# Performance work log

Measured on AMD Instinct MI355X. Metric: run time of the kernel, lower is better.

## Reference

```python
import jax, jax.numpy as jnp
import numpy as np

B, C, H, W = 8, 512, 32, 32
NUM_HEADS = 8
WINDOW = 32
L = H * W
BN_EPS = 1e-5


def setup_inputs() -> dict:
    key = jax.random.key(0)
    ks = jax.random.split(key, 8)
    s = lambda k, shape, sc=0.02: jax.random.normal(k, shape, jnp.float32) * sc
    return {
        "x": jax.random.normal(ks[0], (B, C, H, W), jnp.float32),
        "dw_weight": s(ks[1], (C, 1, 3, 3), 0.1),
        "dw_bias": jnp.zeros((C,), jnp.float32),
        "shared_weight": s(ks[2], (1, 1, 3, 3), 0.3),
        "shared_bias": jnp.zeros((1,), jnp.float32),
        "mix_weight": jnp.float32(0.7),
        "bn_gamma": jnp.ones((C,), jnp.float32),
        "bn_beta": jnp.zeros((C,), jnp.float32),
        "det_w1": s(ks[3], (C // 4, 2 * C)),
        "det_b1": jnp.zeros((C // 4,), jnp.float32),
        "det_w2": s(ks[4], (1, C // 4)),
        "det_b2": jnp.zeros((1,), jnp.float32),
        "in_proj_w": s(ks[5], (3 * C, C)),
        "in_proj_b": jnp.zeros((3 * C,), jnp.float32),
        "out_proj_w": s(ks[6], (C, C)),
        "out_proj_b": jnp.zeros((C,), jnp.float32),
    }


def _circ_pad(x):
    # F.pad(x, (1,1,1,1), mode='circular')
    return jnp.pad(x, ((0, 0), (0, 0), (1, 1), (1, 1)), mode="wrap")


def _dw_conv(xp, w, b):
    # depthwise 3x3, VALID on circularly padded input
    out = jax.lax.conv_general_dilated(
        xp, w, window_strides=(1, 1), padding="VALID",
        dimension_numbers=("NCHW", "OIHW", "NCHW"), feature_group_count=C)
    return out + b[None, :, None, None]


def _local_mask():
    # True = blocked; row i allows columns [i - WINDOW//2, i + WINDOW//2]
    i = jnp.arange(L)[:, None]
    j = jnp.arange(L)[None, :]
    allowed = (j >= i - WINDOW // 2) & (j <= i + WINDOW // 2)
    return ~allowed


def _forward(x, dw_weight, dw_bias, shared_weight, shared_bias, mix_weight,
             bn_gamma, bn_beta, det_w1, det_b1, det_w2, det_b2,
             in_proj_w, in_proj_b, out_proj_w, out_proj_b):
    # --- DualWalze (eval mode: BN uses running_mean=0, running_var=1) ---
    xp = _circ_pad(x)
    main_out = _dw_conv(xp, dw_weight, dw_bias)
    shared_kernel = jnp.broadcast_to(shared_weight, (C, 1, 3, 3))
    shared_b = jnp.broadcast_to(shared_bias, (C,))
    express_out = _dw_conv(xp, shared_kernel, shared_b)
    mix = jax.nn.sigmoid(mix_weight)
    combined = mix * main_out + (1.0 - mix) * express_out + x  # residual
    bn = bn_gamma[None, :, None, None] * combined * jax.lax.rsqrt(jnp.float32(1.0 + BN_EPS)) \
         + bn_beta[None, :, None, None]
    x_walze = jax.nn.gelu(bn, approximate=False)  # (B, C, H, W)

    # --- AdaptiveSpikeDetectorV3 (eval: no history, temp = 1.0) ---
    x_before_seq = x.transpose(0, 2, 3, 1).reshape(B, L, C)
    x_after_seq = x_walze.transpose(0, 2, 3, 1).reshape(B, L, C)
    comb = jnp.concatenate([x_before_seq, x_after_seq], axis=-1)  # (B, L, 2C)
    h = jax.nn.gelu(jnp.einsum("blf,kf->blk", comb, det_w1) + det_b1, approximate=False)
    spike_logits = jnp.einsum("blk,ok->blo", h, det_w2) + det_b2  # (B, L, 1)
    soft_mask = jax.nn.sigmoid(spike_logits)  # temperature 1.0 at progress 0
    soft_mask = soft_mask.reshape(B, H, W, 1).transpose(0, 3, 1, 2)  # (B,1,H,W)

    # --- AttentionWithMemory: windowed MHA over flattened sequence ---
    seq = x_after_seq  # (B, L, C)
    qkv = jnp.einsum("blc,fc->blf", seq, in_proj_w) + in_proj_b
    q, k, v = jnp.split(qkv, 3, axis=-1)
    hd = C // NUM_HEADS
    to_heads = lambda t: t.reshape(B, L, NUM_HEADS, hd).transpose(0, 2, 1, 3)
    q, k, v = to_heads(q), to_heads(k), to_heads(v)
    scores = jnp.einsum("bhqd,bhkd->bhqk", q, k) / jnp.sqrt(jnp.float32(hd))
    scores = jnp.where(_local_mask()[None, None], jnp.float32(-1e30), scores)
    attn = jax.nn.softmax(scores, axis=-1)
    ctx = jnp.einsum("bhqk,bhkd->bhqd", attn, v)
    ctx = ctx.transpose(0, 2, 1, 3).reshape(B, L, C)
    attn_out = jnp.einsum("blc,oc->blo", ctx, out_proj_w) + out_proj_b
    attn_spatial = attn_out.reshape(B, H, W, C).transpose(0, 3, 1, 2)

    # --- gated residual combine ---
    return x_walze + soft_mask * attn_spatial


def reference(x, dw_weight, dw_bias, shared_weight, shared_bias, mix_weight,
              bn_gamma, bn_beta, det_w1, det_b1, det_w2, det_b2,
              in_proj_w, in_proj_b, out_proj_w, out_proj_b):
    return _forward(x, dw_weight, dw_bias, shared_weight, shared_bias, mix_weight,
                    bn_gamma, bn_beta, det_w1, det_b1, det_w2, det_b2,
                    in_proj_w, in_proj_b, out_proj_w, out_proj_b)
```

## Files before the change

kernel.cpp:

```cpp
#include <hip/hip_runtime.h>

#define B_ 8
#define C_ 512
#define H_ 32
#define W_ 32
#define L_ 1024
#define M_ 8192
#define NH_ 8
#define HD_ 64

typedef float f32x4 __attribute__((ext_vector_type(4)));
typedef short s16x8 __attribute__((ext_vector_type(8)));

__device__ __forceinline__ f32x4 mfma_bf16(f32x4 acc, s16x8 a, s16x8 b) {
    asm("v_mfma_f32_16x16x32_bf16 %0, %1, %2, %0" : "+v"(acc) : "v"(a), "v"(b));
    return acc;
}

__device__ __forceinline__ s16x8 ldg8(const unsigned short* p) {
    return *(const s16x8*)p;
}

typedef __attribute__((address_space(1))) const unsigned int glob_u32;
typedef __attribute__((address_space(3))) unsigned int lds_u32;
__device__ __forceinline__ void async_cp16(const void* g, void* l) {
    __builtin_amdgcn_global_load_lds((glob_u32*)g, (lds_u32*)l, 16, 0, 0);
}

__device__ __forceinline__ unsigned short f2bf(float f) {
    unsigned int u = __float_as_uint(f);
    unsigned int r = (u + 0x7FFFu + ((u >> 16) & 1u)) >> 16;
    return (unsigned short)r;
}

__device__ __forceinline__ float bf2f(unsigned short u) {
    return __uint_as_float(((unsigned int)u) << 16);
}

__device__ __forceinline__ float gelu_exact(float v) {
    return 0.5f * v * (1.0f + erff(v * 0.70710678118654752f));
}

__device__ __forceinline__ float sigmoidf_(float v) {
    return 1.0f / (1.0f + __expf(-v));
}

__global__ __launch_bounds__(256) void k_cvt_weights(
        const float* __restrict__ w1, const float* __restrict__ w2,
        const float* __restrict__ w3,
        unsigned short* __restrict__ o1, unsigned short* __restrict__ o2,
        unsigned short* __restrict__ o3, int n1, int n2, int n3) {
    int i = blockIdx.x * 256 + threadIdx.x;
    if (i < n1) o1[i] = f2bf(w1[i]);
    if (i < n2) o2[i] = f2bf(w2[i]);
    if (i < n3) o3[i] = f2bf(w3[i]);
}

__global__ __launch_bounds__(256) void k_walze(
        const float* __restrict__ x, const float* __restrict__ dww,
        const float* __restrict__ dwb, const float* __restrict__ shw,
        const float* __restrict__ shb, const float* __restrict__ mixw,
        const float* __restrict__ gamma, const float* __restrict__ beta,
        float* __restrict__ xw) {
    __shared__ float tile[1024];
    int bc = blockIdx.x;
    int c = bc & (C_ - 1);
    int tid = threadIdx.x;
    const float* xp = x + (size_t)bc * 1024;
#pragma unroll
    for (int t = 0; t < 4; ++t) tile[tid + 256 * t] = xp[tid + 256 * t];
    __syncthreads();
    float wm[9], wsh[9];
#pragma unroll
    for (int t = 0; t < 9; ++t) { wm[t] = dww[c * 9 + t]; wsh[t] = shw[t]; }
    float mix = sigmoidf_(mixw[0]);
    float bmain = dwb[c], bsh = shb[0];
    float g = gamma[c], bt = beta[c];
    const float rs = rsqrtf(1.0f + 1e-5f);
#pragma unroll
    for (int t = 0; t < 4; ++t) {
        int l = tid + 256 * t;
        int h = l >> 5, w = l & 31;
        float accm = 0.f, accs = 0.f;
#pragma unroll
        for (int kh = 0; kh < 3; ++kh) {
            int hh = (h + kh + 31) & 31;
#pragma unroll
            for (int kw = 0; kw < 3; ++kw) {
                int ww = (w + kw + 31) & 31;
                float v = tile[hh * 32 + ww];
                accm += v * wm[kh * 3 + kw];
                accs += v * wsh[kh * 3 + kw];
            }
        }
        float combined = mix * (accm + bmain) + (1.f - mix) * (accs + bsh) + tile[l];
        float bn = g * combined * rs + bt;
        xw[(size_t)bc * 1024 + l] = gelu_exact(bn);
    }
}

__global__ __launch_bounds__(256) void k_pack(
        const float* __restrict__ x, const float* __restrict__ xw,
        unsigned short* __restrict__ comb) {
    __shared__ float Tx[64 * 65];
    __shared__ float Tw[64 * 65];
    int b = blockIdx.z;
    int c0 = blockIdx.y * 64;
    int l0 = blockIdx.x * 64;
    int tid = threadIdx.x;
    for (int idx = tid; idx < 1024; idx += 256) {
        int cr = idx >> 4, f = idx & 15;
        size_t src = ((size_t)(b * C_ + c0 + cr) << 10) + l0 + f * 4;
        float4 vx = *(const float4*)(x + src);
        float4 vw = *(const float4*)(xw + src);
        *(float4*)&Tx[cr * 65 + f * 4] = vx;
        *(float4*)&Tw[cr * 65 + f * 4] = vw;
    }
    __syncthreads();
    for (int idx = tid; idx < 1024; idx += 256) {
        int lr = idx >> 4, f = idx & 15;
        ushort4 ux, uw;
        ux.x = f2bf(Tx[(4 * f + 0) * 65 + lr]);
        ux.y = f2bf(Tx[(4 * f + 1) * 65 + lr]);
        ux.z = f2bf(Tx[(4 * f + 2) * 65 + lr]);
        ux.w = f2bf(Tx[(4 * f + 3) * 65 + lr]);
        uw.x = f2bf(Tw[(4 * f + 0) * 65 + lr]);
        uw.y = f2bf(Tw[(4 * f + 1) * 65 + lr]);
        uw.z = f2bf(Tw[(4 * f + 2) * 65 + lr]);
        uw.w = f2bf(Tw[(4 * f + 3) * 65 + lr]);
        unsigned short* row = comb + (((size_t)(b << 10) + l0 + lr) << 10);
        *(ushort4*)(row + c0 + 4 * f) = ux;
        *(ushort4*)(row + 512 + c0 + 4 * f) = uw;
    }
}

__global__ __launch_bounds__(256) void k_detector(
        const unsigned short* __restrict__ comb, const unsigned short* __restrict__ w1,
        const float* __restrict__ b1, const float* __restrict__ w2,
        const float* __restrict__ b2, float* __restrict__ sm) {
    __shared__ float red[64];
    int tid = threadIdx.x;
    int wave = tid >> 6, lane = tid & 63;
    int col = lane & 15, quad = lane >> 4;
    int m0 = blockIdx.x * 16;
    int koff = quad * 8;
    int nb0 = wave * 32, nb1 = nb0 + 16;
    const unsigned short* pa  = comb + (size_t)(m0 + col) * 1024 + koff;
    const unsigned short* pw0 = w1 + (size_t)(nb0 + col) * 1024 + koff;
    const unsigned short* pw1 = w1 + (size_t)(nb1 + col) * 1024 + koff;
    f32x4 acc0 = {0.f, 0.f, 0.f, 0.f}, acc1 = {0.f, 0.f, 0.f, 0.f};
    for (int k = 0; k < 1024; k += 32) {
        s16x8 a = ldg8(pa + k);
        acc0 = mfma_bf16(acc0, a, ldg8(pw0 + k));
        acc1 = mfma_bf16(acc1, a, ldg8(pw1 + k));
    }
    asm volatile("s_nop 7\ns_nop 7");
    float bia0 = b1[nb0 + col], bia1 = b1[nb1 + col];
    float wv0 = w2[nb0 + col], wv1 = w2[nb1 + col];
#pragma unroll
    for (int r = 0; r < 4; ++r) {
        float h0 = gelu_exact(acc0[r] + bia0);
        float h1 = gelu_exact(acc1[r] + bia1);
        float p = h0 * wv0 + h1 * wv1;
        p += __shfl_xor(p, 1);
        p += __shfl_xor(p, 2);
        p += __shfl_xor(p, 4);
        p += __shfl_xor(p, 8);
        if (col == 0) red[wave * 16 + quad * 4 + r] = p;
    }
    __syncthreads();
    if (tid < 16) {
        float s = red[tid] + red[16 + tid] + red[32 + tid] + red[48 + tid] + b2[0];
        sm[m0 + tid] = sigmoidf_(s);
    }
}

__global__ __launch_bounds__(256) void k_gemm_qkv(
        const unsigned short* __restrict__ A,
        const unsigned short* __restrict__ Wt,
        const float* __restrict__ bias,
        unsigned short* __restrict__ out_hi, unsigned short* __restrict__ out_lo) {
    __shared__ unsigned short As[128 * 64];
    __shared__ unsigned short Bs[128 * 64];
    int tid = threadIdx.x;
    int wave = tid >> 6, lane = tid & 63;
    int col = lane & 15, quad = lane >> 4;
    int wr = wave & 1, wc = wave >> 1;
    int mb = blockIdx.y * 128, nb = blockIdx.x * 128;
    int srow = tid >> 3, sko = tid & 7;
    bool write_lo = (nb >= 1024);
    f32x4 acc[4][4] = {};
    for (int kb = 0; kb < 512; kb += 64) {
#pragma unroll
        for (int p = 0; p < 4; ++p) {
            int r = p * 32 + srow;
            async_cp16(A + (size_t)(mb + r) * 1024 + kb + sko * 8, &As[r * 64 + sko * 8]);
            async_cp16(Wt + (size_t)(nb + r) * 512 + kb + sko * 8, &Bs[r * 64 + sko * 8]);
        }
        __syncthreads();
#pragma unroll
        for (int ks = 0; ks < 64; ks += 32) {
            s16x8 a[4], b[4];
#pragma unroll
            for (int i = 0; i < 4; ++i)
                a[i] = *(const s16x8*)&As[(wr * 64 + i * 16 + col) * 64 + ks + quad * 8];
#pragma unroll
            for (int j = 0; j < 4; ++j)
                b[j] = *(const s16x8*)&Bs[(wc * 64 + j * 16 + col) * 64 + ks + quad * 8];
#pragma unroll
            for (int i = 0; i < 4; ++i)
#pragma unroll
                for (int j = 0; j < 4; ++j)
                    acc[i][j] = mfma_bf16(acc[i][j], a[i], b[j]);
        }
        __syncthreads();
    }
    asm volatile("s_nop 7\ns_nop 7");
#pragma unroll
    for (int i = 0; i < 4; ++i)
#pragma unroll
        for (int j = 0; j < 4; ++j) {
            int n = nb + wc * 64 + j * 16 + col;
            float bv = bias[n];
#pragma unroll
            for (int r = 0; r < 4; ++r) {
                int m = mb + wr * 64 + i * 16 + quad * 4 + r;
                float v = acc[i][j][r] + bv;
                unsigned short hi = f2bf(v);
                size_t idx = (size_t)m * 1536 + n;
                out_hi[idx] = hi;
                if (write_lo) out_lo[idx] = f2bf(v - bf2f(hi));
            }
        }
}

__global__ __launch_bounds__(256) void k_attn(
        const unsigned short* __restrict__ qkv_hi,
        const unsigned short* __restrict__ qkv_lo,
        unsigned short* __restrict__ ctx) {
    __shared__ unsigned short Vth[64 * 112];
    __shared__ unsigned short Vtl[64 * 112];
    __shared__ unsigned short Ph[4][16 * 72];
    __shared__ unsigned short Pl[4][16 * 72];
    int b = blockIdx.z, h = blockIdx.y;
    int q0 = blockIdx.x * 64;
    int tid = threadIdx.x, wave = tid >> 6, lane = tid & 63;
    int col = lane & 15, quad = lane >> 4;
    int jlo_t = max(q0 - 16, 0);
    const unsigned short* baseh = qkv_hi + ((size_t)(b << 10)) * 1536;
    const unsigned short* basel = qkv_lo + ((size_t)(b << 10)) * 1536;
#pragma unroll
    for (int it = 0; it < 3; ++it) {
        int slot = it * 256 + tid;
        int kg = slot >> 6, d = slot & 63;
        int key0 = jlo_t + kg * 8;
        unsigned short eh[8], el[8];
#pragma unroll
        for (int t = 0; t < 8; ++t) {
            size_t ro = (size_t)min(key0 + t, 1023) * 1536 + 1024 + h * 64 + d;
            eh[t] = baseh[ro];
            el[t] = basel[ro];
        }
        ushort4 h0 = {eh[0], eh[1], eh[2], eh[3]}, h1 = {eh[4], eh[5], eh[6], eh[7]};
        ushort4 l0 = {el[0], el[1], el[2], el[3]}, l1 = {el[4], el[5], el[6], el[7]};
        *(ushort4*)&Vth[d * 112 + kg * 8] = h0;
        *(ushort4*)&Vth[d * 112 + kg * 8 + 4] = h1;
        *(ushort4*)&Vtl[d * 112 + kg * 8] = l0;
        *(ushort4*)&Vtl[d * 112 + kg * 8 + 4] = l1;
    }
    {
        int d = tid >> 2, c4 = (tid & 3) * 4;
        ushort4 z = {0, 0, 0, 0};
        *(ushort4*)&Vth[d * 112 + 96 + c4] = z;
        *(ushort4*)&Vtl[d * 112 + 96 + c4] = z;
    }
    __syncthreads();
    int i_min = q0 + wave * 16;
    size_t qoff = (size_t)(i_min + col) * 1536 + h * 64;
    s16x8 aq0h = ldg8(baseh + qoff + quad * 8);
    s16x8 aq1h = ldg8(baseh + qoff + 32 + quad * 8);
    int t0 = (max(i_min - 16, 0) - jlo_t) >> 4;
    int t1 = (min(i_min + 31, 1023) - jlo_t) >> 4;
    f32x4 S[3];
#pragma unroll
    for (int u = 0; u < 3; ++u) {
        int nt = t0 + u;
        size_t koffb = (size_t)min(jlo_t + nt * 16 + col, 1023) * 1536 + 512 + h * 64;
        s16x8 kh0 = ldg8(baseh + koffb + quad * 8);
        s16x8 kh1 = ldg8(baseh + koffb + 32 + quad * 8);
        f32x4 z = {0.f, 0.f, 0.f, 0.f};
        z = mfma_bf16(z, aq0h, kh0);
        z = mfma_bf16(z, aq1h, kh1);
        S[u] = z;
    }
    asm volatile("s_nop 7\ns_nop 7");
    int i_base = i_min + quad * 4;
    float mx[4] = {-1e30f, -1e30f, -1e30f, -1e30f};
#pragma unroll
    for (int u = 0; u < 3; ++u) {
        int nt = t0 + u;
        int j = jlo_t + nt * 16 + col;
        bool live = (nt <= t1);
#pragma unroll
        for (int r = 0; r < 4; ++r) {
            int i = i_base + r;
            bool ok = live && (j <= 1023) && (j >= i - 16) && (j <= i + 16);
            float s = ok ? S[u][r] * 0.125f : -1e30f;
            S[u][r] = s;
            mx[r] = fmaxf(mx[r], s);
        }
    }
#pragma unroll
    for (int r = 0; r < 4; ++r) {
        mx[r] = fmaxf(mx[r], __shfl_xor(mx[r], 1));
        mx[r] = fmaxf(mx[r], __shfl_xor(mx[r], 2));
        mx[r] = fmaxf(mx[r], __shfl_xor(mx[r], 4));
        mx[r] = fmaxf(mx[r], __shfl_xor(mx[r], 8));
    }
    float sum[4] = {0.f, 0.f, 0.f, 0.f};
#pragma unroll
    for (int u = 0; u < 3; ++u)
#pragma unroll
        for (int r = 0; r < 4; ++r) {
            float p = __expf(S[u][r] - mx[r]);
            S[u][r] = p;
            sum[r] += p;
        }
#pragma unroll
    for (int r = 0; r < 4; ++r) {
        sum[r] += __shfl_xor(sum[r], 1);
        sum[r] += __shfl_xor(sum[r], 2);
        sum[r] += __shfl_xor(sum[r], 4);
        sum[r] += __shfl_xor(sum[r], 8);
        sum[r] = 1.f / sum[r];
    }
    int wbase = t0 * 16;
    {
        int pr = lane >> 2, c4 = (lane & 3) * 4;
        ushort4 z = {0, 0, 0, 0};
        *(ushort4*)&Ph[wave][pr * 72 + 48 + c4] = z;
        *(ushort4*)&Pl[wave][pr * 72 + 48 + c4] = z;
    }
#pragma unroll
    for (int u = 0; u < 3; ++u) {
        int pcol = u * 16 + col;
#pragma unroll
        for (int r = 0; r < 4; ++r) {
            float pv = S[u][r] * sum[r];
            unsigned short hi = f2bf(pv);
            Ph[wave][(quad * 4 + r) * 72 + pcol] = hi;
            Pl[wave][(quad * 4 + r) * 72 + pcol] = f2bf(pv - bf2f(hi));
        }
    }
    __syncthreads();
    f32x4 O[4] = {};
#pragma unroll
    for (int ks = 0; ks < 64; ks += 32) {
        s16x8 aph = *(const s16x8*)&Ph[wave][col * 72 + ks + quad * 8];
        s16x8 apl = *(const s16x8*)&Pl[wave][col * 72 + ks + quad * 8];
#pragma unroll
        for (int nt = 0; nt < 4; ++nt) {
            s16x8 bvh = *(const s16x8*)&Vth[(nt * 16 + col) * 112 + wbase + ks + quad * 8];
            s16x8 bvl = *(const s16x8*)&Vtl[(nt * 16 + col) * 112 + wbase + ks + quad * 8];
            O[nt] = mfma_bf16(O[nt], aph, bvh);
            O[nt] = mfma_bf16(O[nt], apl, bvh);
            O[nt] = mfma_bf16(O[nt], aph, bvl);
        }
    }
    asm volatile("s_nop 7\ns_nop 7");
#pragma unroll
    for (int nt = 0; nt < 4; ++nt)
#pragma unroll
        for (int r = 0; r < 4; ++r) {
            int i = i_base + r;
            ctx[((size_t)(b << 10) + i) * 512 + h * 64 + nt * 16 + col] = f2bf(O[nt][r]);
        }
}

__global__ __launch_bounds__(256) void k_out_combine(
        const unsigned short* __restrict__ Wt, const unsigned short* __restrict__ Actx,
        const float* __restrict__ bias, const float* __restrict__ xw,
        const float* __restrict__ sm, float* __restrict__ out) {
    __shared__ unsigned short As[64 * 64];
    __shared__ unsigned short Bs[64 * 64];
    int tid = threadIdx.x;
    int wave = tid >> 6, lane = tid & 63;
    int col = lane & 15, quad = lane >> 4;
    int wr = wave & 1, wc = wave >> 1;
    int mb = blockIdx.y * 64, nb = blockIdx.x * 64;
    int srow = tid >> 3, sko = tid & 7;
    f32x4 acc[2][2] = {};
    for (int kb = 0; kb < 512; kb += 64) {
#pragma unroll
        for (int p = 0; p < 2; ++p) {
            int r = p * 32 + srow;
            async_cp16(Wt + (size_t)(mb + r) * 512 + kb + sko * 8, &As[r * 64 + sko * 8]);
            async_cp16(Actx + (size_t)(nb + r) * 512 + kb + sko * 8, &Bs[r * 64 + sko * 8]);
        }
        __syncthreads();
#pragma unroll
        for (int ks = 0; ks < 64; ks += 32) {
            s16x8 a[2], b[2];
#pragma unroll
            for (int i = 0; i < 2; ++i)
                a[i] = *(const s16x8*)&As[(wr * 32 + i * 16 + col) * 64 + ks + quad * 8];
#pragma unroll
            for (int j = 0; j < 2; ++j)
                b[j] = *(const s16x8*)&Bs[(wc * 32 + j * 16 + col) * 64 + ks + quad * 8];
#pragma unroll
            for (int i = 0; i < 2; ++i)
#pragma unroll
                for (int j = 0; j < 2; ++j)
                    acc[i][j] = mfma_bf16(acc[i][j], a[i], b[j]);
        }
        __syncthreads();
    }
    asm volatile("s_nop 7\ns_nop 7");
#pragma unroll
    for (int i = 0; i < 2; ++i)
#pragma unroll
        for (int j = 0; j < 2; ++j) {
            int seq = nb + wc * 32 + j * 16 + col;
            int bb = seq >> 10, l = seq & 1023;
            float smv = sm[seq];
#pragma unroll
            for (int r = 0; r < 4; ++r) {
                int c = mb + wr * 32 + i * 16 + quad * 4 + r;
                float v = acc[i][j][r] + bias[c];
                size_t oidx = ((size_t)(bb * C_ + c) << 10) + l;
                out[oidx] = xw[oidx] + smv * v;
            }
        }
}

extern "C" void kernel_launch(void* const* d_in, const int* in_sizes, int n_in,
                              void* d_out, int out_size, void* d_ws, size_t ws_size,
                              hipStream_t stream) {
    const float* x      = (const float*)d_in[0];
    const float* dw_w   = (const float*)d_in[1];
    const float* dw_b   = (const float*)d_in[2];
    const float* sh_w   = (const float*)d_in[3];
    const float* sh_b   = (const float*)d_in[4];
    const float* mix_w  = (const float*)d_in[5];
    const float* bn_g   = (const float*)d_in[6];
    const float* bn_b   = (const float*)d_in[7];
    const float* det_w1 = (const float*)d_in[8];
    const float* det_b1 = (const float*)d_in[9];
    const float* det_w2 = (const float*)d_in[10];
    const float* det_b2 = (const float*)d_in[11];
    const float* inp_w  = (const float*)d_in[12];
    const float* inp_b  = (const float*)d_in[13];
    const float* outp_w = (const float*)d_in[14];
    const float* outp_b = (const float*)d_in[15];
    float* out = (float*)d_out;

    char* ws = (char*)d_ws;
    size_t off = 0;
    auto alloc = [&](size_t bytes) -> void* {
        void* p = ws + off;
        off += (bytes + 255) & ~(size_t)255;
        return p;
    };
    float* xw             = (float*)alloc((size_t)M_ * C_ * 4);
    unsigned short* comb  = (unsigned short*)alloc((size_t)M_ * 1024 * 2);
    unsigned short* qkvh  = (unsigned short*)alloc((size_t)M_ * 1536 * 2);
    unsigned short* qkvl  = (unsigned short*)alloc((size_t)M_ * 1536 * 2);
    unsigned short* ctx   = (unsigned short*)alloc((size_t)M_ * 512 * 2);
    float* smask          = (float*)alloc((size_t)M_ * 4);
    unsigned short* w1b   = (unsigned short*)alloc(131072 * 2);
    unsigned short* inwb  = (unsigned short*)alloc(786432 * 2);
    unsigned short* outwb = (unsigned short*)alloc(262144 * 2);
    (void)ws_size; (void)in_sizes; (void)n_in; (void)out_size;

    k_cvt_weights<<<3072, 256, 0, stream>>>(det_w1, inp_w, outp_w, w1b, inwb, outwb,
                                            131072, 786432, 262144);
    k_walze<<<B_ * C_, 256, 0, stream>>>(x, dw_w, dw_b, sh_w, sh_b, mix_w, bn_g, bn_b, xw);
    k_pack<<<dim3(16, 8, 8), 256, 0, stream>>>(x, xw, comb);
    k_detector<<<M_ / 16, 256, 0, stream>>>(comb, w1b, det_b1, det_w2, det_b2, smask);
    k_gemm_qkv<<<dim3(1536 / 128, M_ / 128), 256, 0, stream>>>(comb + 512, inwb, inp_b,
                                                               qkvh, qkvl);
    k_attn<<<dim3(16, NH_, B_), 256, 0, stream>>>(qkvh, qkvl, ctx);
    k_out_combine<<<dim3(M_ / 64, C_ / 64), 256, 0, stream>>>(outwb, ctx, outp_b,
                                                              xw, smask, out);
}
```

Baseline: 187.2 us.

## Fuse weight conversion into walze kernel and merge detector with QKV GEMM

The fp32-to-bf16 weight conversion now runs inside the depthwise-conv (walze) kernel, with each of its 4096 blocks converting a slice of the three weight matrices. The detector MLP and the QKV projection GEMM become one launch whose first 512 blocks do the detector and the remaining 768 do the GEMM tiles. This removes two kernel launches and lets the small detector blocks run alongside the GEMM blocks instead of serialising. In exchange, the walze blocks carry extra global traffic, and the merged kernel reserves the GEMM's LDS for every block, which may limit occupancy for the detector part.

```diff
diff --git a/kernel.cpp b/kernel.cpp
--- a/kernel.cpp
+++ b/kernel.cpp
@@ -45,23 +45,16 @@
     return 1.0f / (1.0f + __expf(-v));
 }
 
-__global__ __launch_bounds__(256) void k_cvt_weights(
-        const float* __restrict__ w1, const float* __restrict__ w2,
-        const float* __restrict__ w3,
-        unsigned short* __restrict__ o1, unsigned short* __restrict__ o2,
-        unsigned short* __restrict__ o3, int n1, int n2, int n3) {
-    int i = blockIdx.x * 256 + threadIdx.x;
-    if (i < n1) o1[i] = f2bf(w1[i]);
-    if (i < n2) o2[i] = f2bf(w2[i]);
-    if (i < n3) o3[i] = f2bf(w3[i]);
-}
-
-__global__ __launch_bounds__(256) void k_walze(
+__global__ __launch_bounds__(256) void k_walze_cvt(
         const float* __restrict__ x, const float* __restrict__ dww,
         const float* __restrict__ dwb, const float* __restrict__ shw,
         const float* __restrict__ shb, const float* __restrict__ mixw,
         const float* __restrict__ gamma, const float* __restrict__ beta,
-        float* __restrict__ xw) {
+        float* __restrict__ xw,
+        const float* __restrict__ w1, const float* __restrict__ w2,
+        const float* __restrict__ w3,
+        unsigned short* __restrict__ o1, unsigned short* __restrict__ o2,
+        unsigned short* __restrict__ o3) {
     __shared__ float tile[1024];
     int bc = blockIdx.x;
     int c = bc & (C_ - 1);
@@ -69,6 +62,16 @@
     const float* xp = x + (size_t)bc * 1024;
 #pragma unroll
     for (int t = 0; t < 4; ++t) tile[tid + 256 * t] = xp[tid + 256 * t];
+    {
+        int g = bc * 256 + tid;
+#pragma unroll
+        for (int t = 0; t < 2; ++t) {
+            int i = g + t * 1048576;
+            if (i < 131072) o1[i] = f2bf(w1[i]);
+            else if (i < 917504) o2[i - 131072] = f2bf(w2[i - 131072]);
+            else if (i < 1179648) o3[i - 917504] = f2bf(w3[i - 917504]);
+        }
+    }
     __syncthreads();
     float wm[9], wsh[9];
 #pragma unroll
@@ -134,104 +137,103 @@
     }
 }
 
-__global__ __launch_bounds__(256) void k_detector(
-        const unsigned short* __restrict__ comb, const unsigned short* __restrict__ w1,
-        const float* __restrict__ b1, const float* __restrict__ w2,
-        const float* __restrict__ b2, float* __restrict__ sm) {
-    __shared__ float red[64];
-    int tid = threadIdx.x;
-    int wave = tid >> 6, lane = tid & 63;
-    int col = lane & 15, quad = lane >> 4;
-    int m0 = blockIdx.x * 16;
-    int koff = quad * 8;
-    int nb0 = wave * 32, nb1 = nb0 + 16;
-    const unsigned short* pa  = comb + (size_t)(m0 + col) * 1024 + koff;
-    const unsigned short* pw0 = w1 + (size_t)(nb0 + col) * 1024 + koff;
-    const unsigned short* pw1 = w1 + (size_t)(nb1 + col) * 1024 + koff;
-    f32x4 acc0 = {0.f, 0.f, 0.f, 0.f}, acc1 = {0.f, 0.f, 0.f, 0.f};
-    for (int k = 0; k < 1024; k += 32) {
-        s16x8 a = ldg8(pa + k);
-        acc0 = mfma_bf16(acc0, a, ldg8(pw0 + k));
-        acc1 = mfma_bf16(acc1, a, ldg8(pw1 + k));
-    }
-    asm volatile("s_nop 7\ns_nop 7");
-    float bia0 = b1[nb0 + col], bia1 = b1[nb1 + col];
-    float wv0 = w2[nb0 + col], wv1 = w2[nb1 + col];
-#pragma unroll
-    for (int r = 0; r < 4; ++r) {
-        float h0 = gelu_exact(acc0[r] + bia0);
-        float h1 = gelu_exact(acc1[r] + bia1);
-        float p = h0 * wv0 + h1 * wv1;
-        p += __shfl_xor(p, 1);
-        p += __shfl_xor(p, 2);
-        p += __shfl_xor(p, 4);
-        p += __shfl_xor(p, 8);
-        if (col == 0) red[wave * 16 + quad * 4 + r] = p;
-    }
-    __syncthreads();
-    if (tid < 16) {
-        float s = red[tid] + red[16 + tid] + red[32 + tid] + red[48 + tid] + b2[0];
-        sm[m0 + tid] = sigmoidf_(s);
-    }
-}
-
-__global__ __launch_bounds__(256) void k_gemm_qkv(
-        const unsigned short* __restrict__ A,
-        const unsigned short* __restrict__ Wt,
-        const float* __restrict__ bias,
+__global__ __launch_bounds__(256) void k_det_qkv(
+        const unsigned short* __restrict__ comb,
+        const unsigned short* __restrict__ w1, const float* __restrict__ b1,
+        const float* __restrict__ w2, const float* __restrict__ b2,
+        float* __restrict__ sm,
+        const unsigned short* __restrict__ Wt, const float* __restrict__ bias,
         unsigned short* __restrict__ out_hi, unsigned short* __restrict__ out_lo) {
     __shared__ unsigned short As[128 * 64];
     __shared__ unsigned short Bs[128 * 64];
     int tid = threadIdx.x;
     int wave = tid >> 6, lane = tid & 63;
     int col = lane & 15, quad = lane >> 4;
-    int wr = wave & 1, wc = wave >> 1;
-    int mb = blockIdx.y * 128, nb = blockIdx.x * 128;
-    int srow = tid >> 3, sko = tid & 7;
-    bool write_lo = (nb >= 1024);
-    f32x4 acc[4][4] = {};
-    for (int kb = 0; kb < 512; kb += 64) {
-#pragma unroll
-        for (int p = 0; p < 4; ++p) {
-            int r = p * 32 + srow;
-            async_cp16(A + (size_t)(mb + r) * 1024 + kb + sko * 8, &As[r * 64 + sko * 8]);
-            async_cp16(Wt + (size_t)(nb + r) * 512 + kb + sko * 8, &Bs[r * 64 + sko * 8]);
+    if (blockIdx.x < 512) {
+        float* red = (float*)As;
+        int m0 = blockIdx.x * 16;
+        int koff = quad * 8;
+        int nb0 = wave * 32, nb1 = nb0 + 16;
+        const unsigned short* pa  = comb + (size_t)(m0 + col) * 1024 + koff;
+        const unsigned short* pw0 = w1 + (size_t)(nb0 + col) * 1024 + koff;
+        const unsigned short* pw1 = w1 + (size_t)(nb1 + col) * 1024 + koff;
+        f32x4 acc0 = {0.f, 0.f, 0.f, 0.f}, acc1 = {0.f, 0.f, 0.f, 0.f};
+        for (int k = 0; k < 1024; k += 32) {
+            s16x8 a = ldg8(pa + k);
+            acc0 = mfma_bf16(acc0, a, ldg8(pw0 + k));
+            acc1 = mfma_bf16(acc1, a, ldg8(pw1 + k));
+        }
+        asm volatile("s_nop 7\ns_nop 7");
+        float bia0 = b1[nb0 + col], bia1 = b1[nb1 + col];
+        float wv0 = w2[nb0 + col], wv1 = w2[nb1 + col];
+#pragma unroll
+        for (int r = 0; r < 4; ++r) {
+            float h0 = gelu_exact(acc0[r] + bia0);
+            float h1 = gelu_exact(acc1[r] + bia1);
+            float p = h0 * wv0 + h1 * wv1;
+            p += __shfl_xor(p, 1);
+            p += __shfl_xor(p, 2);
+            p += __shfl_xor(p, 4);
+            p += __shfl_xor(p, 8);
+            if (col == 0) red[wave * 16 + quad * 4 + r] = p;
         }
         __syncthreads();
-#pragma unroll
-        for (int ks = 0; ks < 64; ks += 32) {
-            s16x8 a[4], b[4];
-#pragma unroll
-            for (int i = 0; i < 4; ++i)
-                a[i] = *(const s16x8*)&As[(wr * 64 + i * 16 + col) * 64 + ks + quad * 8];
-#pragma unroll
-            for (int j = 0; j < 4; ++j)
-                b[j] = *(const s16x8*)&Bs[(wc * 64 + j * 16 + col) * 64 + ks + quad * 8];
-#pragma unroll
-            for (int i = 0; i < 4; ++i)
+        if (tid < 16) {
+            float s = red[tid] + red[16 + tid] + red[32 + tid] + red[48 + tid] + b2[0];
+            sm[m0 + tid] = sigmoidf_(s);
+        }
+    } else {
+        int qbid = blockIdx.x - 512;
+        int nb = (qbid % 12) * 128;
+        int mb = (qbid / 12) * 128;
+        const unsigned short* A = comb + 512;
+        int wr = wave & 1, wc = wave >> 1;
+        int srow = tid >> 3, sko = tid & 7;
+        bool write_lo = (nb >= 1024);
+        f32x4 acc[4][4] = {};
+        for (int kb = 0; kb < 512; kb += 64) {
+#pragma unroll
+            for (int p = 0; p < 4; ++p) {
+                int r = p * 32 + srow;
+                async_cp16(A + (size_t)(mb + r) * 1024 + kb + sko * 8, &As[r * 64 + sko * 8]);
+                async_cp16(Wt + (size_t)(nb + r) * 512 + kb + sko * 8, &Bs[r * 64 + sko * 8]);
+            }
+            __syncthreads();
+#pragma unroll
+            for (int ks = 0; ks < 64; ks += 32) {
+                s16x8 a[4], b[4];
+#pragma unroll
+                for (int i = 0; i < 4; ++i)
+                    a[i] = *(const s16x8*)&As[(wr * 64 + i * 16 + col) * 64 + ks + quad * 8];
 #pragma unroll
                 for (int j = 0; j < 4; ++j)
-                    acc[i][j] = mfma_bf16(acc[i][j], a[i], b[j]);
-        }
-        __syncthreads();
-    }
-    asm volatile("s_nop 7\ns_nop 7");
-#pragma unroll
-    for (int i = 0; i < 4; ++i)
-#pragma unroll
-        for (int j = 0; j < 4; ++j) {
-            int n = nb + wc * 64 + j * 16 + col;
-            float bv = bias[n];
-#pragma unroll
-            for (int r = 0; r < 4; ++r) {
-                int m = mb + wr * 64 + i * 16 + quad * 4 + r;
-                float v = acc[i][j][r] + bv;
-                unsigned short hi = f2bf(v);
-                size_t idx = (size_t)m * 1536 + n;
-                out_hi[idx] = hi;
-                if (write_lo) out_lo[idx] = f2bf(v - bf2f(hi));
+                    b[j] = *(const s16x8*)&Bs[(wc * 64 + j * 16 + col) * 64 + ks + quad * 8];
+#pragma unroll
+                for (int i = 0; i < 4; ++i)
+#pragma unroll
+                    for (int j = 0; j < 4; ++j)
+                        acc[i][j] = mfma_bf16(acc[i][j], a[i], b[j]);
             }
-        }
+            __syncthreads();
+        }
+        asm volatile("s_nop 7\ns_nop 7");
+#pragma unroll
+        for (int i = 0; i < 4; ++i)
+#pragma unroll
+            for (int j = 0; j < 4; ++j) {
+                int n = nb + wc * 64 + j * 16 + col;
+                float bv = bias[n];
+#pragma unroll
+                for (int r = 0; r < 4; ++r) {
+                    int m = mb + wr * 64 + i * 16 + quad * 4 + r;
+                    float v = acc[i][j][r] + bv;
+                    unsigned short hi = f2bf(v);
+                    size_t idx = (size_t)m * 1536 + n;
+                    out_hi[idx] = hi;
+                    if (write_lo) out_lo[idx] = f2bf(v - bf2f(hi));
+                }
+            }
+    }
 }
 
 __global__ __launch_bounds__(256) void k_attn(
@@ -472,13 +474,12 @@
     unsigned short* outwb = (unsigned short*)alloc(262144 * 2);
     (void)ws_size; (void)in_sizes; (void)n_in; (void)out_size;
 
-    k_cvt_weights<<<3072, 256, 0, stream>>>(det_w1, inp_w, outp_w, w1b, inwb, outwb,
-                                            131072, 786432, 262144);
-    k_walze<<<B_ * C_, 256, 0, stream>>>(x, dw_w, dw_b, sh_w, sh_b, mix_w, bn_g, bn_b, xw);
+    k_walze_cvt<<<B_ * C_, 256, 0, stream>>>(x, dw_w, dw_b, sh_w, sh_b, mix_w,
+                                             bn_g, bn_b, xw,
+                                             det_w1, inp_w, outp_w, w1b, inwb, outwb);
     k_pack<<<dim3(16, 8, 8), 256, 0, stream>>>(x, xw, comb);
-    k_detector<<<M_ / 16, 256, 0, stream>>>(comb, w1b, det_b1, det_w2, det_b2, smask);
-    k_gemm_qkv<<<dim3(1536 / 128, M_ / 128), 256, 0, stream>>>(comb + 512, inwb, inp_b,
-                                                               qkvh, qkvl);
+    k_det_qkv<<<512 + 768, 256, 0, stream>>>(comb, w1b, det_b1, det_w2, det_b2, smask,
+                                             inwb, inp_b, qkvh, qkvl);
     k_attn<<<dim3(16, NH_, B_), 256, 0, stream>>>(qkvh, qkvl, ctx);
     k_out_combine<<<dim3(M_ / 64, C_ / 64), 256, 0, stream>>>(outwb, ctx, outp_b,
                                                               xw, smask, out);
```

After: 180.8 us. 1.04x faster.
